# Kernel optimization log

Hardware: AMD Instinct MI355X
Metric: run time of the kernel (lower is better)

The kernel has to match this reference:

```python
import jax, jax.numpy as jnp
import numpy as np

B = 16          # batch (number of point clouds)
N = 16384       # total points across batch
H = 512         # hidden_size
E = 64          # traj_embed_size
T = 8           # max_traj_len
EB = 72         # euler_bins = 360 // 5
OUT = EB * 3 + 2  # action_mlp output: 216 rot logits + open + stop = 218
TEMP = 1.0


def setup_inputs() -> dict:
    key = jax.random.key(0)
    ks = jax.random.split(key, 8)
    rng = np.random.default_rng(0)
    # ragged segment sizes, each >= 256, summing exactly to N
    counts = rng.multinomial(N - B * 256, np.ones(B) / B) + 256
    s = 0.02
    return {
        "point_embeds": jax.random.normal(ks[0], (N, H), jnp.float32),
        "coords": jax.random.normal(ks[1], (N, 3), jnp.float32),
        "traj_emb": jax.random.normal(ks[2], (T, E), jnp.float32) * s,
        "hm_w1": jax.random.normal(ks[3], (H + E, H), jnp.float32) * s,
        "hm_b1": jnp.zeros((H,), jnp.float32),
        "hm_w2": jax.random.normal(ks[4], (H, 4), jnp.float32) * s,
        "hm_b2": jnp.zeros((4,), jnp.float32),
        "act_w1": jax.random.normal(ks[5], (H + E, H), jnp.float32) * s,
        "act_b1": jnp.zeros((H,), jnp.float32),
        "act_w2": jax.random.normal(ks[6], (H, OUT), jnp.float32) * s,
        "act_b2": jnp.zeros((OUT,), jnp.float32),
        "npoints_in_batch": jnp.asarray(counts, jnp.int32),
    }


def _lrelu(x):
    return jnp.where(x >= 0, x, 0.02 * x)


def reference(point_embeds, coords, traj_emb, hm_w1, hm_b1, hm_w2, hm_b2,
              act_w1, act_b1, act_w2, act_b2, npoints_in_batch):
    n = point_embeds.shape[0]
    # segment id per point (replaces torch.split over ragged batch)
    seg = jnp.repeat(jnp.arange(B), npoints_in_batch, total_repeat_length=n)  # (N,)

    # expand with trajectory-step embedding: (N, T, H+E)
    pe = jnp.concatenate([
        jnp.broadcast_to(point_embeds[:, None, :], (n, T, H)),
        jnp.broadcast_to(traj_emb[None, :, :], (n, T, E)),
    ], axis=-1)

    # heatmap MLP: (N, T, 4) = [heatmap logit, delta xyz]
    hm = _lrelu(pe @ hm_w1 + hm_b1) @ hm_w2 + hm_b2
    logits = hm[..., 0]                                # (N, T)

    # per-segment stable softmax over points
    m = jax.ops.segment_max(logits, seg, num_segments=B)          # (B, T)
    e = jnp.exp((logits - m[seg]) / TEMP)                         # (N, T)
    z = jax.ops.segment_sum(e, seg, num_segments=B)               # (B, T)
    h = e / z[seg]                                                # (N, T)

    new_coords = coords[:, None, :] + hm[..., 1:]                 # (N, T, 3)
    xt = jax.ops.segment_sum(h[..., None] * new_coords, seg, num_segments=B)  # (B, T, 3)

    # reduce == 'max': per-segment max pooling of point embeds
    pc = jax.ops.segment_max(pe, seg, num_segments=B)             # (B, T, H+E)
    ae = _lrelu(pc @ act_w1 + act_b1) @ act_w2 + act_b2           # (B, T, 218)

    xr = ae[..., :EB * 3].reshape(B, T, EB, 3)  # euler_disc logits
    xo = ae[..., -2]
    xstop = ae[..., -1]
    return (xt, xr, xo, xstop)
```

## Files before the change

### kernel.cpp

```cpp
#include <hip/hip_runtime.h>
#include <math.h>

typedef unsigned short u16;
typedef unsigned int u32;

#define NPTS 16384
#define HID  512
#define TT   8
#define TE   64
#define NB   16
#define OUTC 218

typedef short s16x8 __attribute__((ext_vector_type(8)));
typedef float f32x4 __attribute__((ext_vector_type(4)));

__device__ __forceinline__ float bf2f(u16 u) {
  return __uint_as_float(((u32)u) << 16);
}
__device__ __forceinline__ u16 f2bf(float f) {
  u32 x = __float_as_uint(f);
  x += 0x7fffu + ((x >> 16) & 1u);
  return (u16)(x >> 16);
}
__device__ __forceinline__ float lrelu(float h) { return fmaxf(h, 0.02f * h); }

__device__ __forceinline__ float rd(const void* p, size_t i, bool f32) {
  return f32 ? ((const float*)p)[i] : bf2f(((const u16*)p)[i]);
}
__device__ __forceinline__ void wr(void* p, size_t i, bool f32, float v) {
  if (f32) ((float*)p)[i] = v;
  else ((u16*)p)[i] = f2bf(v);
}

__device__ __forceinline__ void split_bf16(float x, u16& hi, u16& lo) {
  const u32 xu = __float_as_uint(x);
  hi = (u16)(xu >> 16);
  const float rem = x - __uint_as_float(xu & 0xffff0000u);
  lo = f2bf(rem);
}

__global__ __launch_bounds__(256) void sniff_kernel(const u16* __restrict__ pe,
                                                    int* __restrict__ flag) {
  __shared__ int s;
  const int tid = threadIdx.x;
  if (tid == 0) s = 0;
  __syncthreads();
  int c = 0;
  for (int i = tid; i < 8192; i += 256) {
    const u16 v = pe[i];
    if ((v & 0x7F80u) == 0x7F80u) c = 1;
  }
  if (c) s = 1;
  __syncthreads();
  if (tid == 0) flag[0] = s;
}

__global__ __launch_bounds__(256) void prep_conv_kernel(
    const void* __restrict__ hm_w1, const void* __restrict__ hm_b1,
    const void* __restrict__ traj, const void* __restrict__ hm_w2,
    const void* __restrict__ hm_b2, const void* __restrict__ aw1,
    const void* __restrict__ ab1, float* __restrict__ vprime,
    float* __restrict__ w2f, float* __restrict__ b2f,
    float* __restrict__ avp, u16* __restrict__ Bth, u16* __restrict__ Btl,
    const int* __restrict__ flag) {
  const bool f32 = flag[0] != 0;
  const int tid = threadIdx.x, blk = blockIdx.x;
  if (blk < 8) {
    const int t = blk;
    for (int j = tid; j < 512; j += 256) {
      float acc = rd(hm_b1, j, f32);
      for (int e = 0; e < 64; ++e)
        acc = fmaf(rd(traj, t * 64 + e, f32),
                   rd(hm_w1, (size_t)(512 + e) * 512 + j, f32), acc);
      vprime[t * 512 + j] = acc;
    }
  } else if (blk < 16) {
    const int t = blk - 8;
    for (int j = tid; j < 512; j += 256) {
      float acc = rd(ab1, j, f32);
      for (int e = 0; e < 64; ++e)
        acc = fmaf(rd(traj, t * 64 + e, f32),
                   rd(aw1, (size_t)(512 + e) * 512 + j, f32), acc);
      avp[t * 512 + j] = acc;
    }
  } else if (blk == 16) {
    for (int i = tid; i < 2048; i += 256) w2f[i] = rd(hm_w2, i, f32);
    if (tid < 4) b2f[tid] = rd(hm_b2, tid, f32);
  } else {
    if (!f32) return;
    const float* W1 = (const float*)hm_w1;
    const int g = (blk - 17) * 256 + tid;
    const int j = g & 511;
    const int kbase = (g >> 9) * 8;
    s16x8 hv, lv;
#pragma unroll
    for (int i = 0; i < 8; ++i) {
      u16 h, l;
      split_bf16(W1[(size_t)(kbase + i) * 512 + j], h, l);
      hv[i] = (short)h;
      lv[i] = (short)l;
    }
    const int seg = (j >> 4) * 16 + (kbase >> 5);
    const int lane_ = (((kbase >> 3) & 3) << 4) | (j & 15);
    const size_t dst = ((size_t)seg * 64 + lane_) * 8;
    *(s16x8*)&Bth[dst] = hv;
    *(s16x8*)&Btl[dst] = lv;
  }
}

#define SU_STRIDE 516
__global__ __launch_bounds__(1024, 4) void gemm_fused(
    const float* __restrict__ A, const u16* __restrict__ Bth,
    const u16* __restrict__ Btl, const float* __restrict__ vprime,
    const float* __restrict__ w2f, const float* __restrict__ b2f,
    const float* __restrict__ coords, float* __restrict__ logits,
    float* __restrict__ nc, const int* __restrict__ flag) {
  if (flag[0] == 0) return;
  __shared__ __attribute__((aligned(16))) char smem[64 * SU_STRIDE * 4];
  __shared__ float4 sred[512];
  __shared__ float sW2[2048];
  u16* sAh = (u16*)smem;
  u16* sAl = (u16*)(smem + 65536);
  const int tid = threadIdx.x;
  const int rb = blockIdx.x * 64;
  for (int i = tid; i < 2048; i += 1024) sW2[i] = w2f[i];
#pragma unroll
  for (int it = 0; it < 4; ++it) {
    const int c = tid + it * 1024;
    const int row = ((c >> 10) << 4) | (c & 15);
    const int kc = (((c >> 6) & 15) << 2) | ((c >> 4) & 3);
    const float* src = A + (size_t)(rb + row) * 512 + kc * 8;
    const float4 x0 = *(const float4*)(src);
    const float4 x1 = *(const float4*)(src + 4);
    const float xs[8] = {x0.x, x0.y, x0.z, x0.w, x1.x, x1.y, x1.z, x1.w};
    s16x8 hv, lv;
#pragma unroll
    for (int i = 0; i < 8; ++i) {
      u16 h, l;
      split_bf16(xs[i], h, l);
      hv[i] = (short)h;
      lv[i] = (short)l;
    }
    *(s16x8*)&sAh[c * 8] = hv;
    *(s16x8*)&sAl[c * 8] = lv;
  }
  __syncthreads();
  const int wave = tid >> 6, lane = tid & 63;
  f32x4 acc[4][2];
#pragma unroll
  for (int rt = 0; rt < 4; ++rt)
#pragma unroll
    for (int ct = 0; ct < 2; ++ct) acc[rt][ct] = (f32x4){0.f, 0.f, 0.f, 0.f};
  const int bbase = (wave * 2 * 16 * 64 + lane) * 8;
#define LDB(H, L, ks)                                                          \
  {                                                                            \
    H[0] = *(const s16x8*)&Bth[bbase + (ks) * 512];                            \
    H[1] = *(const s16x8*)&Bth[bbase + 8192 + (ks) * 512];                     \
    L[0] = *(const s16x8*)&Btl[bbase + (ks) * 512];                            \
    L[1] = *(const s16x8*)&Btl[bbase + 8192 + (ks) * 512];                     \
  }
#define LDA(ks)                                                                \
  {                                                                            \
    _Pragma("unroll") for (int rt = 0; rt < 4; ++rt) {                         \
      const int aoff = ((rt * 16 + (ks)) * 64 + lane) * 8;                     \
      ah[rt] = *(const s16x8*)&sAh[aoff];                                      \
      al[rt] = *(const s16x8*)&sAl[aoff];                                      \
    }                                                                          \
  }
#define MM(H, L)                                                               \
  _Pragma("unroll") for (int rt = 0; rt < 4; ++rt)                             \
      _Pragma("unroll") for (int ct = 0; ct < 2; ++ct) {                       \
    acc[rt][ct] = __builtin_amdgcn_mfma_f32_16x16x32_bf16(ah[rt], H[ct],       \
                                                          acc[rt][ct], 0, 0,   \
                                                          0);                  \
    acc[rt][ct] = __builtin_amdgcn_mfma_f32_16x16x32_bf16(ah[rt], L[ct],       \
                                                          acc[rt][ct], 0, 0,   \
                                                          0);                  \
    acc[rt][ct] = __builtin_amdgcn_mfma_f32_16x16x32_bf16(al[rt], H[ct],       \
                                                          acc[rt][ct], 0, 0,   \
                                                          0);                  \
  }
  {
    s16x8 ah[4], al[4];
    s16x8 bh0[2], bl0[2], bh1[2], bl1[2];
    LDB(bh0, bl0, 0);
#pragma unroll
    for (int ks = 0; ks < 16; ks += 2) {
      LDB(bh1, bl1, ks + 1);
      LDA(ks);
      MM(bh0, bl0);
      if (ks + 2 < 16) LDB(bh0, bl0, ks + 2);
      LDA(ks + 1);
      MM(bh1, bl1);
    }
  }
#undef LDB
#undef LDA
#undef MM
  __syncthreads();
  float* sU = (float*)smem;
  const int lr = lane & 15, orow = (lane >> 4) * 4;
#pragma unroll
  for (int rt = 0; rt < 4; ++rt)
#pragma unroll
    for (int ct = 0; ct < 2; ++ct) {
      const int col = (wave * 2 + ct) * 16 + lr;
#pragma unroll
      for (int r = 0; r < 4; ++r)
        sU[(rt * 16 + orow + r) * SU_STRIDE + col] = acc[rt][ct][r];
    }
  __syncthreads();
  const int p = tid & 511, half = tid >> 9;
  const int ln = p >> 3, t = p & 7;
  const int n = rb + ln;
  const float* su = sU + ln * SU_STRIDE + half * 256;
  const float* vp = vprime + t * 512 + half * 256;
  const float4* w4 = (const float4*)sW2 + half * 64 * 4;
  float a0 = 0.f, a1 = 0.f, a2 = 0.f, a3 = 0.f;
#pragma unroll 4
  for (int j4 = 0; j4 < 64; ++j4) {
    const float4 uu = *(const float4*)(su + j4 * 4);
    const float4 vv = *(const float4*)(vp + j4 * 4);
    const float4 w_0 = w4[j4 * 4 + 0];
    const float4 w_1 = w4[j4 * 4 + 1];
    const float4 w_2 = w4[j4 * 4 + 2];
    const float4 w_3 = w4[j4 * 4 + 3];
    float h;
    h = lrelu(uu.x + vv.x);
    a0 = fmaf(h, w_0.x, a0); a1 = fmaf(h, w_0.y, a1);
    a2 = fmaf(h, w_0.z, a2); a3 = fmaf(h, w_0.w, a3);
    h = lrelu(uu.y + vv.y);
    a0 = fmaf(h, w_1.x, a0); a1 = fmaf(h, w_1.y, a1);
    a2 = fmaf(h, w_1.z, a2); a3 = fmaf(h, w_1.w, a3);
    h = lrelu(uu.z + vv.z);
    a0 = fmaf(h, w_2.x, a0); a1 = fmaf(h, w_2.y, a1);
    a2 = fmaf(h, w_2.z, a2); a3 = fmaf(h, w_2.w, a3);
    h = lrelu(uu.w + vv.w);
    a0 = fmaf(h, w_3.x, a0); a1 = fmaf(h, w_3.y, a1);
    a2 = fmaf(h, w_3.z, a2); a3 = fmaf(h, w_3.w, a3);
  }
  if (half) sred[p] = make_float4(a0, a1, a2, a3);
  __syncthreads();
  if (!half) {
    const float4 r = sred[p];
    a0 += r.x; a1 += r.y; a2 += r.z; a3 += r.w;
    logits[(size_t)n * 8 + t] = a0 + b2f[0];
    float* o = nc + ((size_t)n * 8 + t) * 3;
    o[0] = coords[(size_t)n * 3 + 0] + a1 + b2f[1];
    o[1] = coords[(size_t)n * 3 + 1] + a2 + b2f[2];
    o[2] = coords[(size_t)n * 3 + 2] + a3 + b2f[3];
  }
}

#define GR 16
#define KBODY                                                                  \
  _Pragma("unroll") for (int r = 0; r < GR; ++r) {                             \
    const float4 a = *(const float4*)&sA[r * 512 + k];                         \
    acc0[r] = fmaf(a.x, w0[0],                                                 \
              fmaf(a.y, w0[1], fmaf(a.z, w0[2], fmaf(a.w, w0[3], acc0[r])))); \
    acc1[r] = fmaf(a.x, w1[0],                                                 \
              fmaf(a.y, w1[1], fmaf(a.z, w1[2], fmaf(a.w, w1[3], acc1[r])))); \
  }

__global__ __launch_bounds__(256) void gemm_naive(
    const void* __restrict__ A, const void* __restrict__ W1,
    float* __restrict__ U, const int* __restrict__ flag) {
  const bool f32 = flag[0] != 0;
  if (f32) return;
  __shared__ float sA[GR * 512];
  const int tid = threadIdx.x;
  const int rb = blockIdx.x * GR;
  for (int i = tid; i < GR * 512; i += 256) {
    const int r = i >> 9, k = i & 511;
    sA[i] = rd(A, (size_t)(rb + r) * 512 + k, f32);
  }
  __syncthreads();
  const int j0 = tid, j1 = tid + 256;
  float acc0[GR], acc1[GR];
#pragma unroll
  for (int r = 0; r < GR; ++r) { acc0[r] = 0.f; acc1[r] = 0.f; }
  {
    const u16* W = (const u16*)W1;
    for (int k = 0; k < 512; k += 4) {
      float w0[4], w1[4];
#pragma unroll
      for (int kk = 0; kk < 4; ++kk) {
        w0[kk] = bf2f(W[(size_t)(k + kk) * 512 + j0]);
        w1[kk] = bf2f(W[(size_t)(k + kk) * 512 + j1]);
      }
      KBODY
    }
  }
#pragma unroll
  for (int r = 0; r < GR; ++r) {
    U[(size_t)(rb + r) * 512 + j0] = acc0[r];
    U[(size_t)(rb + r) * 512 + j1] = acc1[r];
  }
}

__global__ __launch_bounds__(256) void segmax_kernel(
    const void* __restrict__ pe, const int* __restrict__ npts,
    float* __restrict__ partial, const int* __restrict__ flag) {
  const bool f32 = flag[0] != 0;
  const int blk = blockIdx.x;
  const int b = blk >> 4, c = blk & 15;
  int s0 = 0, cnt = 0;
  for (int i = 0; i < 16; ++i) {
    const int v = npts[i];
    if (i < b) s0 += v;
    if (i == b) cnt = v;
  }
  const int chunk = (cnt + 15) >> 4;
  const int r0 = s0 + c * chunk;
  int r1 = r0 + chunk;
  const int rend = s0 + cnt;
  if (r1 > rend) r1 = rend;
  const int j2 = threadIdx.x;
  float m0 = -1e30f, m1 = -1e30f;
  if (f32) {
    const float* pf = (const float*)pe;
    for (int n = r0; n < r1; ++n) {
      const float2 v = *(const float2*)(pf + (size_t)n * 512 + 2 * j2);
      m0 = fmaxf(m0, v.x);
      m1 = fmaxf(m1, v.y);
    }
  } else {
    const u32* p32 = (const u32*)pe;
    for (int n = r0; n < r1; ++n) {
      const u32 v = p32[(size_t)n * 256 + j2];
      m0 = fmaxf(m0, bf2f((u16)(v & 0xffffu)));
      m1 = fmaxf(m1, bf2f((u16)(v >> 16)));
    }
  }
  partial[(size_t)blk * 512 + 2 * j2] = m0;
  partial[(size_t)blk * 512 + 2 * j2 + 1] = m1;
}

__global__ __launch_bounds__(256) void stage2_kernel(
    const float* __restrict__ U, const float* __restrict__ vprime,
    const float* __restrict__ w2f, const float* __restrict__ b2f,
    const void* __restrict__ coords, float* __restrict__ logits,
    float* __restrict__ nc, const int* __restrict__ flag) {
  const bool f32 = flag[0] != 0;
  if (f32) return;
  __shared__ float s_vp[TT * 512];
  const int tid = threadIdx.x;
  for (int i = tid; i < TT * 512; i += 256) s_vp[i] = vprime[i];
  __syncthreads();
  const int g = (blockIdx.x << 8) + tid;
  const int n = g >> 3, t = g & 7;
  const float4* u4 = (const float4*)(U + (size_t)n * 512);
  const float4* v4 = (const float4*)(s_vp + t * 512);
  const float4* w4 = (const float4*)w2f;
  float a0 = 0.f, a1 = 0.f, a2 = 0.f, a3 = 0.f;
  for (int j4 = 0; j4 < 128; ++j4) {
    const float4 uu = u4[j4];
    const float4 vv = v4[j4];
    const float4 w_0 = w4[j4 * 4 + 0];
    const float4 w_1 = w4[j4 * 4 + 1];
    const float4 w_2 = w4[j4 * 4 + 2];
    const float4 w_3 = w4[j4 * 4 + 3];
    float h;
    h = lrelu(uu.x + vv.x);
    a0 = fmaf(h, w_0.x, a0); a1 = fmaf(h, w_0.y, a1);
    a2 = fmaf(h, w_0.z, a2); a3 = fmaf(h, w_0.w, a3);
    h = lrelu(uu.y + vv.y);
    a0 = fmaf(h, w_1.x, a0); a1 = fmaf(h, w_1.y, a1);
    a2 = fmaf(h, w_1.z, a2); a3 = fmaf(h, w_1.w, a3);
    h = lrelu(uu.z + vv.z);
    a0 = fmaf(h, w_2.x, a0); a1 = fmaf(h, w_2.y, a1);
    a2 = fmaf(h, w_2.z, a2); a3 = fmaf(h, w_2.w, a3);
    h = lrelu(uu.w + vv.w);
    a0 = fmaf(h, w_3.x, a0); a1 = fmaf(h, w_3.y, a1);
    a2 = fmaf(h, w_3.z, a2); a3 = fmaf(h, w_3.w, a3);
  }
  logits[g] = a0 + b2f[0];
  float* o = nc + (size_t)g * 3;
  o[0] = rd(coords, (size_t)n * 3 + 0, f32) + a1 + b2f[1];
  o[1] = rd(coords, (size_t)n * 3 + 1, f32) + a2 + b2f[2];
  o[2] = rd(coords, (size_t)n * 3 + 2, f32) + a3 + b2f[3];
}

__global__ __launch_bounds__(256) void softmax_xt_kernel(
    const float* __restrict__ logits, const float* __restrict__ nc,
    const int* __restrict__ npts, void* __restrict__ out,
    const int* __restrict__ flag) {
  const bool f32 = flag[0] != 0;
  const int b = blockIdx.x >> 3, t = blockIdx.x & 7;
  const int tid = threadIdx.x;
  int s0 = 0, cnt = 0;
  for (int i = 0; i < 16; ++i) {
    const int v = npts[i];
    if (i < b) s0 += v;
    if (i == b) cnt = v;
  }
  __shared__ float wm[4];
  __shared__ float red[4][4];
  float m = -1e30f;
  for (int i = tid; i < cnt; i += 256)
    m = fmaxf(m, logits[(size_t)(s0 + i) * 8 + t]);
#pragma unroll
  for (int o = 32; o > 0; o >>= 1) m = fmaxf(m, __shfl_down(m, o, 64));
  if ((tid & 63) == 0) wm[tid >> 6] = m;
  __syncthreads();
  const float mt = fmaxf(fmaxf(wm[0], wm[1]), fmaxf(wm[2], wm[3]));
  float z = 0.f, x = 0.f, y = 0.f, w = 0.f;
  for (int i = tid; i < cnt; i += 256) {
    const size_t g = (size_t)(s0 + i) * 8 + t;
    const float e = expf(logits[g] - mt);
    const float* c3 = nc + g * 3;
    z += e;
    x = fmaf(e, c3[0], x);
    y = fmaf(e, c3[1], y);
    w = fmaf(e, c3[2], w);
  }
#pragma unroll
  for (int o = 32; o > 0; o >>= 1) {
    z += __shfl_down(z, o, 64);
    x += __shfl_down(x, o, 64);
    y += __shfl_down(y, o, 64);
    w += __shfl_down(w, o, 64);
  }
  if ((tid & 63) == 0) {
    red[0][tid >> 6] = z; red[1][tid >> 6] = x;
    red[2][tid >> 6] = y; red[3][tid >> 6] = w;
  }
  __syncthreads();
  if (tid == 0) {
    const float Z = red[0][0] + red[0][1] + red[0][2] + red[0][3];
    const float X = red[1][0] + red[1][1] + red[1][2] + red[1][3];
    const float Y = red[2][0] + red[2][1] + red[2][2] + red[2][3];
    const float W = red[3][0] + red[3][1] + red[3][2] + red[3][3];
    wr(out, (size_t)(b * 8 + t) * 3 + 0, f32, X / Z);
    wr(out, (size_t)(b * 8 + t) * 3 + 1, f32, Y / Z);
    wr(out, (size_t)(b * 8 + t) * 3 + 2, f32, W / Z);
  }
}

__global__ __launch_bounds__(256) void act_hid_kernel(
    const float* __restrict__ partial, const void* __restrict__ aw1,
    const float* __restrict__ avp, float* __restrict__ hid,
    const int* __restrict__ flag) {
  const bool f32 = flag[0] != 0;
  const int b = blockIdx.x >> 3, jt = blockIdx.x & 7;
  __shared__ float spc[512];
  __shared__ float sred[4][64];
  const int tid = threadIdx.x;
  for (int k = tid; k < 512; k += 256) {
    float m = -1e30f;
#pragma unroll
    for (int c = 0; c < 16; ++c)
      m = fmaxf(m, partial[(size_t)(b * 16 + c) * 512 + k]);
    spc[k] = m;
  }
  __syncthreads();
  const int jj = tid & 63, kq = tid >> 6;
  const int j = jt * 64 + jj;
  const int kb = kq * 128;
  float a0 = 0.f, a1 = 0.f, a2 = 0.f, a3 = 0.f;
  if (f32) {
    const float* W = (const float*)aw1 + (size_t)kb * 512 + j;
#pragma unroll 4
    for (int k = 0; k < 128; k += 4) {
      a0 = fmaf(spc[kb + k + 0], W[(size_t)(k + 0) * 512], a0);
      a1 = fmaf(spc[kb + k + 1], W[(size_t)(k + 1) * 512], a1);
      a2 = fmaf(spc[kb + k + 2], W[(size_t)(k + 2) * 512], a2);
      a3 = fmaf(spc[kb + k + 3], W[(size_t)(k + 3) * 512], a3);
    }
  } else {
    const u16* W = (const u16*)aw1 + (size_t)kb * 512 + j;
#pragma unroll 4
    for (int k = 0; k < 128; k += 4) {
      a0 = fmaf(spc[kb + k + 0], bf2f(W[(size_t)(k + 0) * 512]), a0);
      a1 = fmaf(spc[kb + k + 1], bf2f(W[(size_t)(k + 1) * 512]), a1);
      a2 = fmaf(spc[kb + k + 2], bf2f(W[(size_t)(k + 2) * 512]), a2);
      a3 = fmaf(spc[kb + k + 3], bf2f(W[(size_t)(k + 3) * 512]), a3);
    }
  }
  sred[kq][jj] = (a0 + a1) + (a2 + a3);
  __syncthreads();
  if (kq == 0) {
    const float s = (sred[0][jj] + sred[1][jj]) + (sred[2][jj] + sred[3][jj]);
#pragma unroll
    for (int t = 0; t < 8; ++t)
      hid[(size_t)(b * 8 + t) * 512 + j] = lrelu(s + avp[t * 512 + j]);
  }
}

__global__ __launch_bounds__(256) void act_out_kernel(
    const float* __restrict__ hid, const void* __restrict__ aw2,
    const void* __restrict__ ab2, void* __restrict__ out,
    const int* __restrict__ flag) {
  const bool f32 = flag[0] != 0;
  __shared__ float sh[512];
  const int row = blockIdx.x, tid = threadIdx.x;
  for (int i = tid; i < 512; i += 256) sh[i] = hid[(size_t)row * 512 + i];
  __syncthreads();
  if (tid < OUTC) {
    float a0 = 0.f, a1 = 0.f, a2 = 0.f, a3 = 0.f;
    if (f32) {
      const float* W = (const float*)aw2 + tid;
#pragma unroll 8
      for (int j = 0; j < 512; j += 4) {
        a0 = fmaf(sh[j + 0], W[(size_t)(j + 0) * OUTC], a0);
        a1 = fmaf(sh[j + 1], W[(size_t)(j + 1) * OUTC], a1);
        a2 = fmaf(sh[j + 2], W[(size_t)(j + 2) * OUTC], a2);
        a3 = fmaf(sh[j + 3], W[(size_t)(j + 3) * OUTC], a3);
      }
    } else {
      const u16* W = (const u16*)aw2 + tid;
#pragma unroll 8
      for (int j = 0; j < 512; j += 4) {
        a0 = fmaf(sh[j + 0], bf2f(W[(size_t)(j + 0) * OUTC]), a0);
        a1 = fmaf(sh[j + 1], bf2f(W[(size_t)(j + 1) * OUTC]), a1);
        a2 = fmaf(sh[j + 2], bf2f(W[(size_t)(j + 2) * OUTC]), a2);
        a3 = fmaf(sh[j + 3], bf2f(W[(size_t)(j + 3) * OUTC]), a3);
      }
    }
    const float o = rd(ab2, tid, f32) + ((a0 + a1) + (a2 + a3));
    if (tid < 216)
      wr(out, 384 + (size_t)row * 216 + tid, f32, o);
    else if (tid == 216)
      wr(out, 384 + 27648 + row, f32, o);
    else
      wr(out, 384 + 27648 + 128 + row, f32, o);
  }
}

extern "C" void kernel_launch(void* const* d_in, const int* in_sizes, int n_in,
                              void* d_out, int out_size, void* d_ws,
                              size_t ws_size, hipStream_t stream) {
  (void)in_sizes; (void)n_in; (void)out_size; (void)ws_size;
  const void* pe     = d_in[0];
  const void* coords = d_in[1];
  const void* traj   = d_in[2];
  const void* hm_w1  = d_in[3];
  const void* hm_b1  = d_in[4];
  const void* hm_w2  = d_in[5];
  const void* hm_b2  = d_in[6];
  const void* aw1    = d_in[7];
  const void* ab1    = d_in[8];
  const void* aw2    = d_in[9];
  const void* ab2    = d_in[10];
  const int* npts    = (const int*)d_in[11];

  char* ws = (char*)d_ws;
  int*   flag    = (int*)(ws + 0);
  float* avp     = (float*)(ws + 256);
  float* hid     = (float*)(ws + 16896);
  float* U       = (float*)(ws + 524288);
  float* vprime  = (float*)(ws + 34078720);
  float* w2f     = (float*)(ws + 34095104);
  float* b2f     = (float*)(ws + 34103296);
  float* logits  = (float*)(ws + 34103552);
  float* nc      = (float*)(ws + 34627840);
  float* partial = (float*)(ws + 36200704);
  u16*   Bth     = (u16*)(ws + 524288);
  u16*   Btl     = (u16*)(ws + 524288 + 524288);

  sniff_kernel<<<1, 256, 0, stream>>>((const u16*)pe, flag);
  prep_conv_kernel<<<145, 256, 0, stream>>>(hm_w1, hm_b1, traj, hm_w2, hm_b2,
                                            aw1, ab1, vprime, w2f, b2f, avp,
                                            Bth, Btl, flag);
  gemm_fused<<<NPTS / 64, 1024, 0, stream>>>((const float*)pe, Bth, Btl,
                                             vprime, w2f, b2f,
                                             (const float*)coords, logits, nc,
                                             flag);
  gemm_naive<<<NPTS / GR, 256, 0, stream>>>(pe, hm_w1, U, flag);
  segmax_kernel<<<256, 256, 0, stream>>>(pe, npts, partial, flag);
  stage2_kernel<<<512, 256, 0, stream>>>(U, vprime, w2f, b2f, coords, logits,
                                         nc, flag);
  softmax_xt_kernel<<<128, 256, 0, stream>>>(logits, nc, npts, d_out, flag);
  act_hid_kernel<<<128, 256, 0, stream>>>(partial, aw1, avp, hid, flag);
  act_out_kernel<<<128, 256, 0, stream>>>(hid, aw2, ab2, d_out, flag);
}
```

Measured before the change: 209.0 us.

## Fuse segmax into prep, merge softmax and action-hidden kernels, shrink GEMM tile

Moves the per-segment max pooling into the weight-prep launch and merges the softmax/xt and action-hidden kernels into one launch, cutting the kernel count from nine to five. The fused MFMA GEMM now handles 32 rows per block, which doubles the grid and raises occupancy, and its epilogue is split four ways across threads with a rotated index. It also adds a single-pass bf16 MFMA path that replaces the naive bf16 GEMM and stage2 kernels. The trade-off is some extra branching and a smaller per-block tile that gives less reuse of the B operand.

```diff
diff --git a/kernel.cpp b/kernel.cpp
--- a/kernel.cpp
+++ b/kernel.cpp
@@ -59,10 +59,11 @@
     const void* __restrict__ hm_w1, const void* __restrict__ hm_b1,
     const void* __restrict__ traj, const void* __restrict__ hm_w2,
     const void* __restrict__ hm_b2, const void* __restrict__ aw1,
-    const void* __restrict__ ab1, float* __restrict__ vprime,
+    const void* __restrict__ ab1, const void* __restrict__ pe,
+    const int* __restrict__ npts, float* __restrict__ vprime,
     float* __restrict__ w2f, float* __restrict__ b2f,
     float* __restrict__ avp, u16* __restrict__ Bth, u16* __restrict__ Btl,
-    const int* __restrict__ flag) {
+    float* __restrict__ partial, const int* __restrict__ flag) {
   const bool f32 = flag[0] != 0;
   const int tid = threadIdx.x, blk = blockIdx.x;
   if (blk < 8) {
@@ -86,69 +87,110 @@
   } else if (blk == 16) {
     for (int i = tid; i < 2048; i += 256) w2f[i] = rd(hm_w2, i, f32);
     if (tid < 4) b2f[tid] = rd(hm_b2, tid, f32);
-  } else {
-    if (!f32) return;
-    const float* W1 = (const float*)hm_w1;
+  } else if (blk < 145) {
     const int g = (blk - 17) * 256 + tid;
     const int j = g & 511;
     const int kbase = (g >> 9) * 8;
-    s16x8 hv, lv;
-#pragma unroll
-    for (int i = 0; i < 8; ++i) {
-      u16 h, l;
-      split_bf16(W1[(size_t)(kbase + i) * 512 + j], h, l);
-      hv[i] = (short)h;
-      lv[i] = (short)l;
-    }
     const int seg = (j >> 4) * 16 + (kbase >> 5);
     const int lane_ = (((kbase >> 3) & 3) << 4) | (j & 15);
     const size_t dst = ((size_t)seg * 64 + lane_) * 8;
-    *(s16x8*)&Bth[dst] = hv;
-    *(s16x8*)&Btl[dst] = lv;
-  }
-}
-
-#define SU_STRIDE 516
-__global__ __launch_bounds__(1024, 4) void gemm_fused(
-    const float* __restrict__ A, const u16* __restrict__ Bth,
+    s16x8 hv, lv;
+    if (f32) {
+      const float* W1 = (const float*)hm_w1;
+#pragma unroll
+      for (int i = 0; i < 8; ++i) {
+        u16 h, l;
+        split_bf16(W1[(size_t)(kbase + i) * 512 + j], h, l);
+        hv[i] = (short)h;
+        lv[i] = (short)l;
+      }
+      *(s16x8*)&Bth[dst] = hv;
+      *(s16x8*)&Btl[dst] = lv;
+    } else {
+      const u16* W1 = (const u16*)hm_w1;
+#pragma unroll
+      for (int i = 0; i < 8; ++i) hv[i] = (short)W1[(size_t)(kbase + i) * 512 + j];
+      *(s16x8*)&Bth[dst] = hv;
+    }
+  } else {
+    const int blk2 = blk - 145;
+    const int b = blk2 >> 4, c = blk2 & 15;
+    int s0 = 0, cnt = 0;
+    for (int i = 0; i < 16; ++i) {
+      const int v = npts[i];
+      if (i < b) s0 += v;
+      if (i == b) cnt = v;
+    }
+    const int chunk = (cnt + 15) >> 4;
+    const int r0 = s0 + c * chunk;
+    int r1 = r0 + chunk;
+    const int rend = s0 + cnt;
+    if (r1 > rend) r1 = rend;
+    const int j2 = tid;
+    float m0 = -1e30f, m1 = -1e30f;
+    if (f32) {
+      const float* pf = (const float*)pe;
+      for (int n = r0; n < r1; ++n) {
+        const float2 v = *(const float2*)(pf + (size_t)n * 512 + 2 * j2);
+        m0 = fmaxf(m0, v.x);
+        m1 = fmaxf(m1, v.y);
+      }
+    } else {
+      const u32* p32 = (const u32*)pe;
+      for (int n = r0; n < r1; ++n) {
+        const u32 v = p32[(size_t)n * 256 + j2];
+        m0 = fmaxf(m0, bf2f((u16)(v & 0xffffu)));
+        m1 = fmaxf(m1, bf2f((u16)(v >> 16)));
+      }
+    }
+    partial[(size_t)blk2 * 512 + 2 * j2] = m0;
+    partial[(size_t)blk2 * 512 + 2 * j2 + 1] = m1;
+  }
+}
+
+__global__ __launch_bounds__(1024, 8) void gemm_fused(
+    const void* __restrict__ A, const u16* __restrict__ Bth,
     const u16* __restrict__ Btl, const float* __restrict__ vprime,
     const float* __restrict__ w2f, const float* __restrict__ b2f,
-    const float* __restrict__ coords, float* __restrict__ logits,
+    const void* __restrict__ coords, float* __restrict__ logits,
     float* __restrict__ nc, const int* __restrict__ flag) {
-  if (flag[0] == 0) return;
-  __shared__ __attribute__((aligned(16))) char smem[64 * SU_STRIDE * 4];
-  __shared__ float4 sred[512];
-  __shared__ float sW2[2048];
+  const bool f32 = flag[0] != 0;
+  __shared__ __attribute__((aligned(16))) char smem[32 * 512 * 4];
+  __shared__ float4 sred[3][256];
   u16* sAh = (u16*)smem;
-  u16* sAl = (u16*)(smem + 65536);
+  u16* sAl = (u16*)(smem + 32768);
   const int tid = threadIdx.x;
-  const int rb = blockIdx.x * 64;
-  for (int i = tid; i < 2048; i += 1024) sW2[i] = w2f[i];
-#pragma unroll
-  for (int it = 0; it < 4; ++it) {
+  const int rb = blockIdx.x * 32;
+#pragma unroll
+  for (int it = 0; it < 2; ++it) {
     const int c = tid + it * 1024;
     const int row = ((c >> 10) << 4) | (c & 15);
     const int kc = (((c >> 6) & 15) << 2) | ((c >> 4) & 3);
-    const float* src = A + (size_t)(rb + row) * 512 + kc * 8;
-    const float4 x0 = *(const float4*)(src);
-    const float4 x1 = *(const float4*)(src + 4);
-    const float xs[8] = {x0.x, x0.y, x0.z, x0.w, x1.x, x1.y, x1.z, x1.w};
-    s16x8 hv, lv;
-#pragma unroll
-    for (int i = 0; i < 8; ++i) {
-      u16 h, l;
-      split_bf16(xs[i], h, l);
-      hv[i] = (short)h;
-      lv[i] = (short)l;
-    }
-    *(s16x8*)&sAh[c * 8] = hv;
-    *(s16x8*)&sAl[c * 8] = lv;
+    if (f32) {
+      const float* src = (const float*)A + (size_t)(rb + row) * 512 + kc * 8;
+      const float4 x0 = *(const float4*)(src);
+      const float4 x1 = *(const float4*)(src + 4);
+      const float xs[8] = {x0.x, x0.y, x0.z, x0.w, x1.x, x1.y, x1.z, x1.w};
+      s16x8 hv, lv;
+#pragma unroll
+      for (int i = 0; i < 8; ++i) {
+        u16 h, l;
+        split_bf16(xs[i], h, l);
+        hv[i] = (short)h;
+        lv[i] = (short)l;
+      }
+      *(s16x8*)&sAh[c * 8] = hv;
+      *(s16x8*)&sAl[c * 8] = lv;
+    } else {
+      const u16* src = (const u16*)A + (size_t)(rb + row) * 512 + kc * 8;
+      *(s16x8*)&sAh[c * 8] = *(const s16x8*)src;
+    }
   }
   __syncthreads();
   const int wave = tid >> 6, lane = tid & 63;
-  f32x4 acc[4][2];
-#pragma unroll
-  for (int rt = 0; rt < 4; ++rt)
+  f32x4 acc[2][2];
+#pragma unroll
+  for (int rt = 0; rt < 2; ++rt)
 #pragma unroll
     for (int ct = 0; ct < 2; ++ct) acc[rt][ct] = (f32x4){0.f, 0.f, 0.f, 0.f};
   const int bbase = (wave * 2 * 16 * 64 + lane) * 8;
@@ -161,14 +203,14 @@
   }
 #define LDA(ks)                                                                \
   {                                                                            \
-    _Pragma("unroll") for (int rt = 0; rt < 4; ++rt) {                         \
+    _Pragma("unroll") for (int rt = 0; rt < 2; ++rt) {                         \
       const int aoff = ((rt * 16 + (ks)) * 64 + lane) * 8;                     \
       ah[rt] = *(const s16x8*)&sAh[aoff];                                      \
       al[rt] = *(const s16x8*)&sAl[aoff];                                      \
     }                                                                          \
   }
-#define MM(H, L)                                                               \
-  _Pragma("unroll") for (int rt = 0; rt < 4; ++rt)                             \
+#define MM3(H, L)                                                              \
+  _Pragma("unroll") for (int rt = 0; rt < 2; ++rt)                             \
       _Pragma("unroll") for (int ct = 0; ct < 2; ++ct) {                       \
     acc[rt][ct] = __builtin_amdgcn_mfma_f32_16x16x32_bf16(ah[rt], H[ct],       \
                                                           acc[rt][ct], 0, 0,   \
@@ -180,51 +222,68 @@
                                                           acc[rt][ct], 0, 0,   \
                                                           0);                  \
   }
-  {
-    s16x8 ah[4], al[4];
+  if (f32) {
+    s16x8 ah[2], al[2];
     s16x8 bh0[2], bl0[2], bh1[2], bl1[2];
     LDB(bh0, bl0, 0);
 #pragma unroll
     for (int ks = 0; ks < 16; ks += 2) {
       LDB(bh1, bl1, ks + 1);
       LDA(ks);
-      MM(bh0, bl0);
+      MM3(bh0, bl0);
       if (ks + 2 < 16) LDB(bh0, bl0, ks + 2);
       LDA(ks + 1);
-      MM(bh1, bl1);
+      MM3(bh1, bl1);
+    }
+  } else {
+    s16x8 ah[2], bh[2];
+#pragma unroll
+    for (int ks = 0; ks < 16; ++ks) {
+      bh[0] = *(const s16x8*)&Bth[bbase + ks * 512];
+      bh[1] = *(const s16x8*)&Bth[bbase + 8192 + ks * 512];
+#pragma unroll
+      for (int rt = 0; rt < 2; ++rt)
+        ah[rt] = *(const s16x8*)&sAh[((rt * 16 + ks) * 64 + lane) * 8];
+#pragma unroll
+      for (int rt = 0; rt < 2; ++rt)
+#pragma unroll
+        for (int ct = 0; ct < 2; ++ct)
+          acc[rt][ct] = __builtin_amdgcn_mfma_f32_16x16x32_bf16(
+              ah[rt], bh[ct], acc[rt][ct], 0, 0, 0);
     }
   }
 #undef LDB
 #undef LDA
-#undef MM
+#undef MM3
   __syncthreads();
   float* sU = (float*)smem;
   const int lr = lane & 15, orow = (lane >> 4) * 4;
 #pragma unroll
-  for (int rt = 0; rt < 4; ++rt)
+  for (int rt = 0; rt < 2; ++rt)
 #pragma unroll
     for (int ct = 0; ct < 2; ++ct) {
       const int col = (wave * 2 + ct) * 16 + lr;
 #pragma unroll
       for (int r = 0; r < 4; ++r)
-        sU[(rt * 16 + orow + r) * SU_STRIDE + col] = acc[rt][ct][r];
-    }
-  __syncthreads();
-  const int p = tid & 511, half = tid >> 9;
+        sU[(rt * 16 + orow + r) * 512 + col] = acc[rt][ct][r];
+    }
+  __syncthreads();
+  const int p = tid & 255, q = tid >> 8;
   const int ln = p >> 3, t = p & 7;
   const int n = rb + ln;
-  const float* su = sU + ln * SU_STRIDE + half * 256;
-  const float* vp = vprime + t * 512 + half * 256;
-  const float4* w4 = (const float4*)sW2 + half * 64 * 4;
+  const float* su = sU + ln * 512;
+  const float* vp = vprime + t * 512;
+  const float4* w4 = (const float4*)w2f;
   float a0 = 0.f, a1 = 0.f, a2 = 0.f, a3 = 0.f;
 #pragma unroll 4
-  for (int j4 = 0; j4 < 64; ++j4) {
-    const float4 uu = *(const float4*)(su + j4 * 4);
-    const float4 vv = *(const float4*)(vp + j4 * 4);
-    const float4 w_0 = w4[j4 * 4 + 0];
-    const float4 w_1 = w4[j4 * 4 + 1];
-    const float4 w_2 = w4[j4 * 4 + 2];
-    const float4 w_3 = w4[j4 * 4 + 3];
+  for (int i = 0; i < 32; ++i) {
+    const int jj = q * 32 + ((i + ln) & 31);
+    const float4 uu = *(const float4*)(su + jj * 4);
+    const float4 vv = *(const float4*)(vp + jj * 4);
+    const float4 w_0 = w4[jj * 4 + 0];
+    const float4 w_1 = w4[jj * 4 + 1];
+    const float4 w_2 = w4[jj * 4 + 2];
+    const float4 w_3 = w4[jj * 4 + 3];
     float h;
     h = lrelu(uu.x + vv.x);
     a0 = fmaf(h, w_0.x, a0); a1 = fmaf(h, w_0.y, a1);
@@ -239,251 +298,123 @@
     a0 = fmaf(h, w_3.x, a0); a1 = fmaf(h, w_3.y, a1);
     a2 = fmaf(h, w_3.z, a2); a3 = fmaf(h, w_3.w, a3);
   }
-  if (half) sred[p] = make_float4(a0, a1, a2, a3);
-  __syncthreads();
-  if (!half) {
-    const float4 r = sred[p];
-    a0 += r.x; a1 += r.y; a2 += r.z; a3 += r.w;
+  if (q) sred[q - 1][p] = make_float4(a0, a1, a2, a3);
+  __syncthreads();
+  if (!q) {
+#pragma unroll
+    for (int s = 0; s < 3; ++s) {
+      const float4 r = sred[s][p];
+      a0 += r.x; a1 += r.y; a2 += r.z; a3 += r.w;
+    }
     logits[(size_t)n * 8 + t] = a0 + b2f[0];
     float* o = nc + ((size_t)n * 8 + t) * 3;
-    o[0] = coords[(size_t)n * 3 + 0] + a1 + b2f[1];
-    o[1] = coords[(size_t)n * 3 + 1] + a2 + b2f[2];
-    o[2] = coords[(size_t)n * 3 + 2] + a3 + b2f[3];
-  }
-}
-
-#define GR 16
-#define KBODY                                                                  \
-  _Pragma("unroll") for (int r = 0; r < GR; ++r) {                             \
-    const float4 a = *(const float4*)&sA[r * 512 + k];                         \
-    acc0[r] = fmaf(a.x, w0[0],                                                 \
-              fmaf(a.y, w0[1], fmaf(a.z, w0[2], fmaf(a.w, w0[3], acc0[r])))); \
-    acc1[r] = fmaf(a.x, w1[0],                                                 \
-              fmaf(a.y, w1[1], fmaf(a.z, w1[2], fmaf(a.w, w1[3], acc1[r])))); \
-  }
-
-__global__ __launch_bounds__(256) void gemm_naive(
-    const void* __restrict__ A, const void* __restrict__ W1,
-    float* __restrict__ U, const int* __restrict__ flag) {
-  const bool f32 = flag[0] != 0;
-  if (f32) return;
-  __shared__ float sA[GR * 512];
-  const int tid = threadIdx.x;
-  const int rb = blockIdx.x * GR;
-  for (int i = tid; i < GR * 512; i += 256) {
-    const int r = i >> 9, k = i & 511;
-    sA[i] = rd(A, (size_t)(rb + r) * 512 + k, f32);
-  }
-  __syncthreads();
-  const int j0 = tid, j1 = tid + 256;
-  float acc0[GR], acc1[GR];
-#pragma unroll
-  for (int r = 0; r < GR; ++r) { acc0[r] = 0.f; acc1[r] = 0.f; }
-  {
-    const u16* W = (const u16*)W1;
-    for (int k = 0; k < 512; k += 4) {
-      float w0[4], w1[4];
-#pragma unroll
-      for (int kk = 0; kk < 4; ++kk) {
-        w0[kk] = bf2f(W[(size_t)(k + kk) * 512 + j0]);
-        w1[kk] = bf2f(W[(size_t)(k + kk) * 512 + j1]);
-      }
-      KBODY
-    }
-  }
-#pragma unroll
-  for (int r = 0; r < GR; ++r) {
-    U[(size_t)(rb + r) * 512 + j0] = acc0[r];
-    U[(size_t)(rb + r) * 512 + j1] = acc1[r];
-  }
-}
-
-__global__ __launch_bounds__(256) void segmax_kernel(
-    const void* __restrict__ pe, const int* __restrict__ npts,
-    float* __restrict__ partial, const int* __restrict__ flag) {
-  const bool f32 = flag[0] != 0;
-  const int blk = blockIdx.x;
-  const int b = blk >> 4, c = blk & 15;
-  int s0 = 0, cnt = 0;
-  for (int i = 0; i < 16; ++i) {
-    const int v = npts[i];
-    if (i < b) s0 += v;
-    if (i == b) cnt = v;
-  }
-  const int chunk = (cnt + 15) >> 4;
-  const int r0 = s0 + c * chunk;
-  int r1 = r0 + chunk;
-  const int rend = s0 + cnt;
-  if (r1 > rend) r1 = rend;
-  const int j2 = threadIdx.x;
-  float m0 = -1e30f, m1 = -1e30f;
-  if (f32) {
-    const float* pf = (const float*)pe;
-    for (int n = r0; n < r1; ++n) {
-      const float2 v = *(const float2*)(pf + (size_t)n * 512 + 2 * j2);
-      m0 = fmaxf(m0, v.x);
-      m1 = fmaxf(m1, v.y);
-    }
-  } else {
-    const u32* p32 = (const u32*)pe;
-    for (int n = r0; n < r1; ++n) {
-      const u32 v = p32[(size_t)n * 256 + j2];
-      m0 = fmaxf(m0, bf2f((u16)(v & 0xffffu)));
-      m1 = fmaxf(m1, bf2f((u16)(v >> 16)));
-    }
-  }
-  partial[(size_t)blk * 512 + 2 * j2] = m0;
-  partial[(size_t)blk * 512 + 2 * j2 + 1] = m1;
-}
-
-__global__ __launch_bounds__(256) void stage2_kernel(
-    const float* __restrict__ U, const float* __restrict__ vprime,
-    const float* __restrict__ w2f, const float* __restrict__ b2f,
-    const void* __restrict__ coords, float* __restrict__ logits,
-    float* __restrict__ nc, const int* __restrict__ flag) {
-  const bool f32 = flag[0] != 0;
-  if (f32) return;
-  __shared__ float s_vp[TT * 512];
-  const int tid = threadIdx.x;
-  for (int i = tid; i < TT * 512; i += 256) s_vp[i] = vprime[i];
-  __syncthreads();
-  const int g = (blockIdx.x << 8) + tid;
-  const int n = g >> 3, t = g & 7;
-  const float4* u4 = (const float4*)(U + (size_t)n * 512);
-  const float4* v4 = (const float4*)(s_vp + t * 512);
-  const float4* w4 = (const float4*)w2f;
-  float a0 = 0.f, a1 = 0.f, a2 = 0.f, a3 = 0.f;
-  for (int j4 = 0; j4 < 128; ++j4) {
-    const float4 uu = u4[j4];
-    const float4 vv = v4[j4];
-    const float4 w_0 = w4[j4 * 4 + 0];
-    const float4 w_1 = w4[j4 * 4 + 1];
-    const float4 w_2 = w4[j4 * 4 + 2];
-    const float4 w_3 = w4[j4 * 4 + 3];
-    float h;
-    h = lrelu(uu.x + vv.x);
-    a0 = fmaf(h, w_0.x, a0); a1 = fmaf(h, w_0.y, a1);
-    a2 = fmaf(h, w_0.z, a2); a3 = fmaf(h, w_0.w, a3);
-    h = lrelu(uu.y + vv.y);
-    a0 = fmaf(h, w_1.x, a0); a1 = fmaf(h, w_1.y, a1);
-    a2 = fmaf(h, w_1.z, a2); a3 = fmaf(h, w_1.w, a3);
-    h = lrelu(uu.z + vv.z);
-    a0 = fmaf(h, w_2.x, a0); a1 = fmaf(h, w_2.y, a1);
-    a2 = fmaf(h, w_2.z, a2); a3 = fmaf(h, w_2.w, a3);
-    h = lrelu(uu.w + vv.w);
-    a0 = fmaf(h, w_3.x, a0); a1 = fmaf(h, w_3.y, a1);
-    a2 = fmaf(h, w_3.z, a2); a3 = fmaf(h, w_3.w, a3);
-  }
-  logits[g] = a0 + b2f[0];
-  float* o = nc + (size_t)g * 3;
-  o[0] = rd(coords, (size_t)n * 3 + 0, f32) + a1 + b2f[1];
-  o[1] = rd(coords, (size_t)n * 3 + 1, f32) + a2 + b2f[2];
-  o[2] = rd(coords, (size_t)n * 3 + 2, f32) + a3 + b2f[3];
-}
-
-__global__ __launch_bounds__(256) void softmax_xt_kernel(
+    o[0] = rd(coords, (size_t)n * 3 + 0, f32) + a1 + b2f[1];
+    o[1] = rd(coords, (size_t)n * 3 + 1, f32) + a2 + b2f[2];
+    o[2] = rd(coords, (size_t)n * 3 + 2, f32) + a3 + b2f[3];
+  }
+}
+
+__global__ __launch_bounds__(256) void softact_kernel(
     const float* __restrict__ logits, const float* __restrict__ nc,
-    const int* __restrict__ npts, void* __restrict__ out,
+    const int* __restrict__ npts, const float* __restrict__ partial,
+    const void* __restrict__ aw1, const float* __restrict__ avp,
+    float* __restrict__ hid, void* __restrict__ out,
     const int* __restrict__ flag) {
   const bool f32 = flag[0] != 0;
-  const int b = blockIdx.x >> 3, t = blockIdx.x & 7;
   const int tid = threadIdx.x;
-  int s0 = 0, cnt = 0;
-  for (int i = 0; i < 16; ++i) {
-    const int v = npts[i];
-    if (i < b) s0 += v;
-    if (i == b) cnt = v;
-  }
-  __shared__ float wm[4];
-  __shared__ float red[4][4];
-  float m = -1e30f;
-  for (int i = tid; i < cnt; i += 256)
-    m = fmaxf(m, logits[(size_t)(s0 + i) * 8 + t]);
-#pragma unroll
-  for (int o = 32; o > 0; o >>= 1) m = fmaxf(m, __shfl_down(m, o, 64));
-  if ((tid & 63) == 0) wm[tid >> 6] = m;
-  __syncthreads();
-  const float mt = fmaxf(fmaxf(wm[0], wm[1]), fmaxf(wm[2], wm[3]));
-  float z = 0.f, x = 0.f, y = 0.f, w = 0.f;
-  for (int i = tid; i < cnt; i += 256) {
-    const size_t g = (size_t)(s0 + i) * 8 + t;
-    const float e = expf(logits[g] - mt);
-    const float* c3 = nc + g * 3;
-    z += e;
-    x = fmaf(e, c3[0], x);
-    y = fmaf(e, c3[1], y);
-    w = fmaf(e, c3[2], w);
-  }
-#pragma unroll
-  for (int o = 32; o > 0; o >>= 1) {
-    z += __shfl_down(z, o, 64);
-    x += __shfl_down(x, o, 64);
-    y += __shfl_down(y, o, 64);
-    w += __shfl_down(w, o, 64);
-  }
-  if ((tid & 63) == 0) {
-    red[0][tid >> 6] = z; red[1][tid >> 6] = x;
-    red[2][tid >> 6] = y; red[3][tid >> 6] = w;
-  }
-  __syncthreads();
-  if (tid == 0) {
-    const float Z = red[0][0] + red[0][1] + red[0][2] + red[0][3];
-    const float X = red[1][0] + red[1][1] + red[1][2] + red[1][3];
-    const float Y = red[2][0] + red[2][1] + red[2][2] + red[2][3];
-    const float W = red[3][0] + red[3][1] + red[3][2] + red[3][3];
-    wr(out, (size_t)(b * 8 + t) * 3 + 0, f32, X / Z);
-    wr(out, (size_t)(b * 8 + t) * 3 + 1, f32, Y / Z);
-    wr(out, (size_t)(b * 8 + t) * 3 + 2, f32, W / Z);
-  }
-}
-
-__global__ __launch_bounds__(256) void act_hid_kernel(
-    const float* __restrict__ partial, const void* __restrict__ aw1,
-    const float* __restrict__ avp, float* __restrict__ hid,
-    const int* __restrict__ flag) {
-  const bool f32 = flag[0] != 0;
-  const int b = blockIdx.x >> 3, jt = blockIdx.x & 7;
-  __shared__ float spc[512];
-  __shared__ float sred[4][64];
-  const int tid = threadIdx.x;
-  for (int k = tid; k < 512; k += 256) {
+  if (blockIdx.x < 128) {
+    const int b = blockIdx.x >> 3, t = blockIdx.x & 7;
+    int s0 = 0, cnt = 0;
+    for (int i = 0; i < 16; ++i) {
+      const int v = npts[i];
+      if (i < b) s0 += v;
+      if (i == b) cnt = v;
+    }
+    __shared__ float wm[4];
+    __shared__ float red[4][4];
     float m = -1e30f;
-#pragma unroll
-    for (int c = 0; c < 16; ++c)
-      m = fmaxf(m, partial[(size_t)(b * 16 + c) * 512 + k]);
-    spc[k] = m;
-  }
-  __syncthreads();
-  const int jj = tid & 63, kq = tid >> 6;
-  const int j = jt * 64 + jj;
-  const int kb = kq * 128;
-  float a0 = 0.f, a1 = 0.f, a2 = 0.f, a3 = 0.f;
-  if (f32) {
-    const float* W = (const float*)aw1 + (size_t)kb * 512 + j;
+    for (int i = tid; i < cnt; i += 256)
+      m = fmaxf(m, logits[(size_t)(s0 + i) * 8 + t]);
+#pragma unroll
+    for (int o = 32; o > 0; o >>= 1) m = fmaxf(m, __shfl_down(m, o, 64));
+    if ((tid & 63) == 0) wm[tid >> 6] = m;
+    __syncthreads();
+    const float mt = fmaxf(fmaxf(wm[0], wm[1]), fmaxf(wm[2], wm[3]));
+    float z = 0.f, x = 0.f, y = 0.f, w = 0.f;
+    for (int i = tid; i < cnt; i += 256) {
+      const size_t g = (size_t)(s0 + i) * 8 + t;
+      const float e = expf(logits[g] - mt);
+      const float* c3 = nc + g * 3;
+      z += e;
+      x = fmaf(e, c3[0], x);
+      y = fmaf(e, c3[1], y);
+      w = fmaf(e, c3[2], w);
+    }
+#pragma unroll
+    for (int o = 32; o > 0; o >>= 1) {
+      z += __shfl_down(z, o, 64);
+      x += __shfl_down(x, o, 64);
+      y += __shfl_down(y, o, 64);
+      w += __shfl_down(w, o, 64);
+    }
+    if ((tid & 63) == 0) {
+      red[0][tid >> 6] = z; red[1][tid >> 6] = x;
+      red[2][tid >> 6] = y; red[3][tid >> 6] = w;
+    }
+    __syncthreads();
+    if (tid == 0) {
+      const float Z = red[0][0] + red[0][1] + red[0][2] + red[0][3];
+      const float X = red[1][0] + red[1][1] + red[1][2] + red[1][3];
+      const float Y = red[2][0] + red[2][1] + red[2][2] + red[2][3];
+      const float W = red[3][0] + red[3][1] + red[3][2] + red[3][3];
+      wr(out, (size_t)(b * 8 + t) * 3 + 0, f32, X / Z);
+      wr(out, (size_t)(b * 8 + t) * 3 + 1, f32, Y / Z);
+      wr(out, (size_t)(b * 8 + t) * 3 + 2, f32, W / Z);
+    }
+  } else {
+    const int blk2 = blockIdx.x - 128;
+    const int b = blk2 >> 3, jt = blk2 & 7;
+    __shared__ float spc[512];
+    __shared__ float sred2[4][64];
+    for (int k = tid; k < 512; k += 256) {
+      float m = -1e30f;
+#pragma unroll
+      for (int c = 0; c < 16; ++c)
+        m = fmaxf(m, partial[(size_t)(b * 16 + c) * 512 + k]);
+      spc[k] = m;
+    }
+    __syncthreads();
+    const int jj = tid & 63, kq = tid >> 6;
+    const int j = jt * 64 + jj;
+    const int kb = kq * 128;
+    float a0 = 0.f, a1 = 0.f, a2 = 0.f, a3 = 0.f;
+    if (f32) {
+      const float* W = (const float*)aw1 + (size_t)kb * 512 + j;
 #pragma unroll 4
-    for (int k = 0; k < 128; k += 4) {
-      a0 = fmaf(spc[kb + k + 0], W[(size_t)(k + 0) * 512], a0);
-      a1 = fmaf(spc[kb + k + 1], W[(size_t)(k + 1) * 512], a1);
-      a2 = fmaf(spc[kb + k + 2], W[(size_t)(k + 2) * 512], a2);
-      a3 = fmaf(spc[kb + k + 3], W[(size_t)(k + 3) * 512], a3);
-    }
-  } else {
-    const u16* W = (const u16*)aw1 + (size_t)kb * 512 + j;
+      for (int k = 0; k < 128; k += 4) {
+        a0 = fmaf(spc[kb + k + 0], W[(size_t)(k + 0) * 512], a0);
+        a1 = fmaf(spc[kb + k + 1], W[(size_t)(k + 1) * 512], a1);
+        a2 = fmaf(spc[kb + k + 2], W[(size_t)(k + 2) * 512], a2);
+        a3 = fmaf(spc[kb + k + 3], W[(size_t)(k + 3) * 512], a3);
+      }
+    } else {
+      const u16* W = (const u16*)aw1 + (size_t)kb * 512 + j;
 #pragma unroll 4
-    for (int k = 0; k < 128; k += 4) {
-      a0 = fmaf(spc[kb + k + 0], bf2f(W[(size_t)(k + 0) * 512]), a0);
-      a1 = fmaf(spc[kb + k + 1], bf2f(W[(size_t)(k + 1) * 512]), a1);
-      a2 = fmaf(spc[kb + k + 2], bf2f(W[(size_t)(k + 2) * 512]), a2);
-      a3 = fmaf(spc[kb + k + 3], bf2f(W[(size_t)(k + 3) * 512]), a3);
-    }
-  }
-  sred[kq][jj] = (a0 + a1) + (a2 + a3);
-  __syncthreads();
-  if (kq == 0) {
-    const float s = (sred[0][jj] + sred[1][jj]) + (sred[2][jj] + sred[3][jj]);
-#pragma unroll
-    for (int t = 0; t < 8; ++t)
-      hid[(size_t)(b * 8 + t) * 512 + j] = lrelu(s + avp[t * 512 + j]);
+      for (int k = 0; k < 128; k += 4) {
+        a0 = fmaf(spc[kb + k + 0], bf2f(W[(size_t)(k + 0) * 512]), a0);
+        a1 = fmaf(spc[kb + k + 1], bf2f(W[(size_t)(k + 1) * 512]), a1);
+        a2 = fmaf(spc[kb + k + 2], bf2f(W[(size_t)(k + 2) * 512]), a2);
+        a3 = fmaf(spc[kb + k + 3], bf2f(W[(size_t)(k + 3) * 512]), a3);
+      }
+    }
+    sred2[kq][jj] = (a0 + a1) + (a2 + a3);
+    __syncthreads();
+    if (kq == 0) {
+      const float s = (sred2[0][jj] + sred2[1][jj]) + (sred2[2][jj] + sred2[3][jj]);
+#pragma unroll
+      for (int t = 0; t < 8; ++t)
+        hid[(size_t)(b * 8 + t) * 512 + j] = lrelu(s + avp[t * 512 + j]);
+    }
   }
 }
 
@@ -548,29 +479,22 @@
   int*   flag    = (int*)(ws + 0);
   float* avp     = (float*)(ws + 256);
   float* hid     = (float*)(ws + 16896);
-  float* U       = (float*)(ws + 524288);
+  u16*   Bth     = (u16*)(ws + 524288);
+  u16*   Btl     = (u16*)(ws + 1048576);
   float* vprime  = (float*)(ws + 34078720);
   float* w2f     = (float*)(ws + 34095104);
   float* b2f     = (float*)(ws + 34103296);
   float* logits  = (float*)(ws + 34103552);
   float* nc      = (float*)(ws + 34627840);
   float* partial = (float*)(ws + 36200704);
-  u16*   Bth     = (u16*)(ws + 524288);
-  u16*   Btl     = (u16*)(ws + 524288 + 524288);
 
   sniff_kernel<<<1, 256, 0, stream>>>((const u16*)pe, flag);
-  prep_conv_kernel<<<145, 256, 0, stream>>>(hm_w1, hm_b1, traj, hm_w2, hm_b2,
-                                            aw1, ab1, vprime, w2f, b2f, avp,
-                                            Bth, Btl, flag);
-  gemm_fused<<<NPTS / 64, 1024, 0, stream>>>((const float*)pe, Bth, Btl,
-                                             vprime, w2f, b2f,
-                                             (const float*)coords, logits, nc,
-                                             flag);
-  gemm_naive<<<NPTS / GR, 256, 0, stream>>>(pe, hm_w1, U, flag);
-  segmax_kernel<<<256, 256, 0, stream>>>(pe, npts, partial, flag);
-  stage2_kernel<<<512, 256, 0, stream>>>(U, vprime, w2f, b2f, coords, logits,
-                                         nc, flag);
-  softmax_xt_kernel<<<128, 256, 0, stream>>>(logits, nc, npts, d_out, flag);
-  act_hid_kernel<<<128, 256, 0, stream>>>(partial, aw1, avp, hid, flag);
+  prep_conv_kernel<<<401, 256, 0, stream>>>(hm_w1, hm_b1, traj, hm_w2, hm_b2,
+                                            aw1, ab1, pe, npts, vprime, w2f,
+                                            b2f, avp, Bth, Btl, partial, flag);
+  gemm_fused<<<NPTS / 32, 1024, 0, stream>>>(pe, Bth, Btl, vprime, w2f, b2f,
+                                             coords, logits, nc, flag);
+  softact_kernel<<<256, 256, 0, stream>>>(logits, nc, npts, partial, aw1, avp,
+                                          hid, d_out, flag);
   act_out_kernel<<<128, 256, 0, stream>>>(hid, aw2, ab2, d_out, flag);
 }
```

Result: slower. 217.3 us (+4.0%).
